# Kernel tuning notes

Hardware: AMD Instinct MI355X
Metric: run time of the kernel (lower is better)

The kernel has to match this reference:

```python
import jax, jax.numpy as jnp
import numpy as np

B, H, W, C = 16, 56, 56, 384
WS, SHIFT, NH = 8, 4, 12
HID = 4 * C
N = WS * WS
EPS = 1e-5


def _rel_index():
    coords = np.stack(np.meshgrid(np.arange(WS), np.arange(WS), indexing='ij')).reshape(2, -1)
    rel = coords[:, :, None] - coords[:, None, :]
    rel = rel.transpose(1, 2, 0).astype(np.int32)
    rel[..., 0] += WS - 1
    rel[..., 1] += WS - 1
    rel[..., 0] *= 2 * WS - 1
    return rel.sum(-1)  # [N, N]


def _attn_mask():
    img = np.zeros((H, W))
    bounds = [(0, H - WS), (H - WS, H - SHIFT), (H - SHIFT, H)]
    cnt = 0
    for h0, h1 in bounds:
        for w0, w1 in bounds:
            img[h0:h1, w0:w1] = cnt
            cnt += 1
    mw = img.reshape(H // WS, WS, W // WS, WS).transpose(0, 2, 1, 3).reshape(-1, N)
    am = mw[:, None, :] - mw[:, :, None]
    return np.where(am != 0, -100.0, 0.0).astype(np.float32)  # [nW, N, N]


def setup_inputs() -> dict:
    key = jax.random.key(0)
    ks = jax.random.split(key, 12)
    s = lambda k, shp, sc=0.02: (jax.random.normal(k, shp, jnp.float32) * sc)
    return {
        'x': jax.random.normal(ks[0], (B, H * W, C), jnp.float32),
        'norm1_g': jnp.ones((C,), jnp.float32),
        'norm1_b': jnp.zeros((C,), jnp.float32),
        'qkv_w': s(ks[1], (C, 3 * C)),
        'qkv_b': jnp.zeros((3 * C,), jnp.float32),
        'proj_w': s(ks[2], (C, C)),
        'proj_b': jnp.zeros((C,), jnp.float32),
        'rel_bias': s(ks[3], ((2 * WS - 1) * (2 * WS - 1), NH)),
        'norm2_g': jnp.ones((C,), jnp.float32),
        'norm2_b': jnp.zeros((C,), jnp.float32),
        'fc1_w': s(ks[4], (C, HID)),
        'fc1_b': jnp.zeros((HID,), jnp.float32),
        'fc2_w': s(ks[5], (HID, C)),
        'fc2_b': jnp.zeros((C,), jnp.float32),
        'rel_index': jnp.asarray(_rel_index()),
        'attn_mask': jnp.asarray(_attn_mask()),
    }


def _ln(x, g, b):
    mu = x.mean(-1, keepdims=True)
    var = ((x - mu) ** 2).mean(-1, keepdims=True)
    return (x - mu) * jax.lax.rsqrt(var + EPS) * g + b


def reference(x, norm1_g, norm1_b, qkv_w, qkv_b, proj_w, proj_b, rel_bias,
              norm2_g, norm2_b, fc1_w, fc1_b, fc2_w, fc2_b, rel_index, attn_mask):
    hd = C // NH
    scale = hd ** -0.5
    shortcut = x
    h = _ln(x, norm1_g, norm1_b).reshape(B, H, W, C)
    h = jnp.roll(h, (-SHIFT, -SHIFT), axis=(1, 2))
    # window partition -> [B*nW, N, C]
    xw = h.reshape(B, H // WS, WS, W // WS, WS, C).transpose(0, 1, 3, 2, 4, 5).reshape(-1, N, C)
    B_ = xw.shape[0]
    qkv = (xw @ qkv_w + qkv_b).reshape(B_, N, 3, NH, hd).transpose(2, 0, 3, 1, 4)
    q, k, v = qkv[0], qkv[1], qkv[2]  # [B_, NH, N, hd]
    attn = jnp.einsum('bhid,bhjd->bhij', q * scale, k)
    bias = rel_bias[rel_index.reshape(-1)].reshape(N, N, NH).transpose(2, 0, 1)  # [NH, N, N]
    attn = attn + bias[None]
    nW = attn_mask.shape[0]
    attn = attn.reshape(B_ // nW, nW, NH, N, N) + attn_mask[None, :, None]
    attn = attn.reshape(B_, NH, N, N)
    attn = jax.nn.softmax(attn, axis=-1)
    out = jnp.einsum('bhij,bhjd->bhid', attn, v).transpose(0, 2, 1, 3).reshape(B_, N, C)
    out = out @ proj_w + proj_b
    # window reverse
    out = out.reshape(B, H // WS, W // WS, WS, WS, C).transpose(0, 1, 3, 2, 4, 5).reshape(B, H, W, C)
    out = jnp.roll(out, (SHIFT, SHIFT), axis=(1, 2)).reshape(B, H * W, C)
    y = shortcut + out
    h2 = _ln(y, norm2_g, norm2_b)
    mlp = jax.nn.gelu(h2 @ fc1_w + fc1_b, approximate=False) @ fc2_w + fc2_b
    y = y + mlp
    return (y, attn)
```

## Files before the change

kernel.cpp:

```cpp
#include <hip/hip_runtime.h>
#include <hip/hip_bf16.h>
#include <math.h>

#define ROWS 50176

typedef short s16;
typedef unsigned int u32;
typedef __attribute__((ext_vector_type(4))) float f32x4;
typedef __attribute__((ext_vector_type(8))) short s16x8;
typedef __attribute__((ext_vector_type(8))) __bf16 bf16x8;

typedef __attribute__((address_space(1))) const u32 gu32;
typedef __attribute__((address_space(3))) u32 lu32;

__device__ __forceinline__ void gload16(const void* g, void* l) {
  __builtin_amdgcn_global_load_lds((gu32*)g, (lu32*)l, 16, 0, 0);
}

__device__ __forceinline__ s16 f2bf(float f) {
  unsigned u = __float_as_uint(f);
  u = (u + 0x7fffu + ((u >> 16) & 1u)) >> 16;
  return (s16)u;
}

__global__ void convT(const float* __restrict__ src, s16* __restrict__ dst, int K, int N) {
  int i = blockIdx.x * 256 + threadIdx.x;
  if (i >= K * N) return;
  int n = i / K, k = i - n * K;
  dst[i] = f2bf(src[(size_t)k * N + n]);
}

__global__ __launch_bounds__(256) void ln_k(const float* __restrict__ x,
    const float* __restrict__ g, const float* __restrict__ b,
    s16* __restrict__ out, int window_map) {
  int r = blockIdx.x * 4 + (threadIdx.x >> 6);
  int lane = threadIdx.x & 63;
  size_t src;
  if (window_map) {
    int w = r >> 6, t = r & 63;
    int bb = w / 49, wi = w - bb * 49;
    int wh = wi / 7, ww = wi - wh * 7;
    int i = (wh * 8 + (t >> 3) + 4) % 56;
    int j = (ww * 8 + (t & 7) + 4) % 56;
    src = (size_t)bb * 3136 + i * 56 + j;
  } else {
    src = (size_t)r;
  }
  const float* xr = x + src * 384;
  float v[6];
  float s = 0.f;
#pragma unroll
  for (int e = 0; e < 6; ++e) { v[e] = xr[lane + e * 64]; s += v[e]; }
#pragma unroll
  for (int o = 1; o < 64; o <<= 1) s += __shfl_xor(s, o, 64);
  float mu = s * (1.f / 384.f);
  float q = 0.f;
#pragma unroll
  for (int e = 0; e < 6; ++e) { float d = v[e] - mu; q += d * d; }
#pragma unroll
  for (int o = 1; o < 64; o <<= 1) q += __shfl_xor(q, o, 64);
  float rs = rsqrtf(q * (1.f / 384.f) + 1e-5f);
  s16* orow = out + (size_t)r * 384;
#pragma unroll
  for (int e = 0; e < 6; ++e) {
    int c = lane + e * 64;
    orow[c] = f2bf((v[e] - mu) * rs * g[c] + b[c]);
  }
}

template<int EPI>
__global__ __launch_bounds__(256) void gemm_bt(const s16* __restrict__ A,
    const s16* __restrict__ BT, const float* __restrict__ bias, int K, int N,
    s16* __restrict__ obf, float* of, const float* res) {
  __shared__ s16 Asm[128 * 64];
  __shared__ s16 Bsm[128 * 64];
  const int t = threadIdx.x;
  const int nbx = N >> 7;
  const int nwg = gridDim.x;
  {
  }
  int id = blockIdx.x;
  const int q8 = nwg >> 3, r8 = nwg & 7;
  const int xcd = id & 7, loc = id >> 3;
  const int swz = (xcd < r8 ? xcd * (q8 + 1) : r8 * (q8 + 1) + (xcd - r8) * q8) + loc;
  const int by = swz / nbx, bx = swz - by * nbx;
  const int m0 = by * 128, n0 = bx * 128;

  const int wv = t >> 6, lane = t & 63;
  const int wr = wv >> 1, wc = wv & 1;
  const int lr = lane & 15, lg = lane >> 4;

  const s16* asrc[4]; const s16* bsrc[4];
  char* adst[4]; char* bdst[4];
#pragma unroll
  for (int i = 0; i < 4; ++i) {
    int o = (i * 256 + t) * 16;
    int row = o >> 7, pc = (o >> 4) & 7, lc = pc ^ (row & 7);
    asrc[i] = A + (size_t)(m0 + row) * K + lc * 8;
    adst[i] = (char*)Asm + o;
    bsrc[i] = BT + (size_t)(n0 + row) * K + lc * 8;
    bdst[i] = (char*)Bsm + o;
  }

  f32x4 acc[4][4] = {};

  for (int k0 = 0; k0 < K; k0 += 64) {
#pragma unroll
    for (int i = 0; i < 4; ++i) {
      gload16(asrc[i] + k0, adst[i]);
      gload16(bsrc[i] + k0, bdst[i]);
    }
    __syncthreads();
    bf16x8 af[2][4], bv[2][4];
#pragma unroll
    for (int kk = 0; kk < 2; ++kk) {
      const int cb = ((kk << 2) | lg) ^ (lr & 7);
#pragma unroll
      for (int m = 0; m < 4; ++m) {
        af[kk][m] = *reinterpret_cast<const bf16x8*>(
            (const char*)Asm + (wr * 64 + m * 16 + lr) * 128 + cb * 16);
        bv[kk][m] = *reinterpret_cast<const bf16x8*>(
            (const char*)Bsm + (wc * 64 + m * 16 + lr) * 128 + cb * 16);
      }
    }
#pragma unroll
    for (int kk = 0; kk < 2; ++kk)
#pragma unroll
      for (int m = 0; m < 4; ++m)
#pragma unroll
        for (int n = 0; n < 4; ++n)
          acc[m][n] = __builtin_amdgcn_mfma_f32_16x16x32_bf16(af[kk][m], bv[kk][n], acc[m][n], 0, 0, 0);
    __syncthreads();
  }

#pragma unroll
  for (int m = 0; m < 4; ++m) {
#pragma unroll
    for (int r = 0; r < 4; ++r) {
      const int row = m0 + wr * 64 + m * 16 + lg * 4 + r;
      size_t drow = (size_t)row;
      if (EPI == 1) {
        int w = row >> 6, tt = row & 63;
        int bb = w / 49, wi = w - bb * 49;
        int wh = wi / 7, ww = wi - wh * 7;
        int fi = (wh * 8 + (tt >> 3) + 4) % 56;
        int fj = (ww * 8 + (tt & 7) + 4) % 56;
        drow = (size_t)bb * 3136 + fi * 56 + fj;
      }
#pragma unroll
      for (int n = 0; n < 4; ++n) {
        const int col = n0 + wc * 64 + n * 16 + lr;
        float v = acc[m][n][r] + bias[col];
        if (EPI == 0) {
          obf[(size_t)row * N + col] = f2bf(v);
        } else if (EPI == 1) {
          size_t o = drow * 384 + col;
          of[o] = res[o] + v;
        } else if (EPI == 2) {
          v = 0.5f * v * (1.f + erff(v * 0.70710678118f));
          obf[(size_t)row * N + col] = f2bf(v);
        } else {
          size_t o = (size_t)row * 384 + col;
          of[o] = res[o] + v;
        }
      }
    }
  }
}

__global__ __launch_bounds__(64) void attn_k(const s16* __restrict__ qkv,
    const float* __restrict__ rel_bias, const int* __restrict__ rel_index,
    const float* __restrict__ mask, float* __restrict__ probs, s16* __restrict__ aout) {
  __shared__ s16 VT[32][72];
  __shared__ s16 P[64][72];
  const int blk = blockIdx.x;
  const int w = blk / 12, nh = blk - w * 12;
  const int lane = threadIdx.x;
  const int lr = lane & 15, lg = lane >> 4;
  const s16* base = qkv + (size_t)w * 64 * 1152;

  {
    const s16* vrow = base + (size_t)lane * 1152 + 768 + nh * 32;
    s16x8 v0 = *reinterpret_cast<const s16x8*>(vrow);
    s16x8 v1 = *reinterpret_cast<const s16x8*>(vrow + 8);
    s16x8 v2 = *reinterpret_cast<const s16x8*>(vrow + 16);
    s16x8 v3 = *reinterpret_cast<const s16x8*>(vrow + 24);
#pragma unroll
    for (int d = 0; d < 8; ++d) {
      VT[d][lane] = v0[d];
      VT[8 + d][lane] = v1[d];
      VT[16 + d][lane] = v2[d];
      VT[24 + d][lane] = v3[d];
    }
  }

  bf16x8 qf[4], kf[4];
#pragma unroll
  for (int m = 0; m < 4; ++m)
    qf[m] = *reinterpret_cast<const bf16x8*>(base + (size_t)(m * 16 + lr) * 1152 + nh * 32 + lg * 8);
#pragma unroll
  for (int n = 0; n < 4; ++n)
    kf[n] = *reinterpret_cast<const bf16x8*>(base + (size_t)(n * 16 + lr) * 1152 + 384 + nh * 32 + lg * 8);

  f32x4 s[4][4] = {};
#pragma unroll
  for (int m = 0; m < 4; ++m)
#pragma unroll
    for (int n = 0; n < 4; ++n)
      s[m][n] = __builtin_amdgcn_mfma_f32_16x16x32_bf16(qf[m], kf[n], s[m][n], 0, 0, 0);

  const float scale = 0.1767766952966369f;
  const float* mrow = mask + (size_t)(w % 49) * 4096;
#pragma unroll
  for (int m = 0; m < 4; ++m)
#pragma unroll
    for (int n = 0; n < 4; ++n)
#pragma unroll
      for (int r = 0; r < 4; ++r) {
        int i = m * 16 + lg * 4 + r, j = n * 16 + lr;
        s[m][n][r] = s[m][n][r] * scale
                   + rel_bias[(size_t)rel_index[i * 64 + j] * 12 + nh]
                   + mrow[i * 64 + j];
      }
#pragma unroll
  for (int m = 0; m < 4; ++m)
#pragma unroll
    for (int r = 0; r < 4; ++r) {
      float mx = fmaxf(fmaxf(s[m][0][r], s[m][1][r]), fmaxf(s[m][2][r], s[m][3][r]));
#pragma unroll
      for (int o = 1; o < 16; o <<= 1) mx = fmaxf(mx, __shfl_xor(mx, o, 64));
      float sum = 0.f;
#pragma unroll
      for (int n = 0; n < 4; ++n) {
        float e = __expf(s[m][n][r] - mx);
        s[m][n][r] = e;
        sum += e;
      }
#pragma unroll
      for (int o = 1; o < 16; o <<= 1) sum += __shfl_xor(sum, o, 64);
      float inv = 1.f / sum;
#pragma unroll
      for (int n = 0; n < 4; ++n) s[m][n][r] *= inv;
    }
  float* prow = probs + (size_t)(w * 12 + nh) * 4096;
#pragma unroll
  for (int m = 0; m < 4; ++m)
#pragma unroll
    for (int n = 0; n < 4; ++n)
#pragma unroll
      for (int r = 0; r < 4; ++r) {
        int i = m * 16 + lg * 4 + r, j = n * 16 + lr;
        float pv = s[m][n][r];
        prow[i * 64 + j] = pv;
        P[i][j] = f2bf(pv);
      }
  __syncthreads();
  f32x4 o2[4][2] = {};
#pragma unroll
  for (int m = 0; m < 4; ++m)
#pragma unroll
    for (int kk = 0; kk < 2; ++kk) {
      bf16x8 pa = *reinterpret_cast<const bf16x8*>(&P[m * 16 + lr][kk * 32 + lg * 8]);
#pragma unroll
      for (int n = 0; n < 2; ++n) {
        bf16x8 vb = *reinterpret_cast<const bf16x8*>(&VT[n * 16 + lr][kk * 32 + lg * 8]);
        o2[m][n] = __builtin_amdgcn_mfma_f32_16x16x32_bf16(pa, vb, o2[m][n], 0, 0, 0);
      }
    }
#pragma unroll
  for (int m = 0; m < 4; ++m)
#pragma unroll
    for (int n = 0; n < 2; ++n)
#pragma unroll
      for (int r = 0; r < 4; ++r) {
        int i = m * 16 + lg * 4 + r, d = n * 16 + lr;
        aout[((size_t)w * 64 + i) * 384 + nh * 32 + d] = f2bf(o2[m][n][r]);
      }
}

extern "C" void kernel_launch(void* const* d_in, const int* in_sizes, int n_in,
                              void* d_out, int out_size, void* d_ws, size_t ws_size,
                              hipStream_t stream) {
  const float* x        = (const float*)d_in[0];
  const float* n1g      = (const float*)d_in[1];
  const float* n1b      = (const float*)d_in[2];
  const float* qkv_w    = (const float*)d_in[3];
  const float* qkv_b    = (const float*)d_in[4];
  const float* proj_w   = (const float*)d_in[5];
  const float* proj_b   = (const float*)d_in[6];
  const float* rel_bias = (const float*)d_in[7];
  const float* n2g      = (const float*)d_in[8];
  const float* n2b      = (const float*)d_in[9];
  const float* fc1_w    = (const float*)d_in[10];
  const float* fc1_b    = (const float*)d_in[11];
  const float* fc2_w    = (const float*)d_in[12];
  const float* fc2_b    = (const float*)d_in[13];
  const int*   rel_idx  = (const int*)d_in[14];
  const float* amask    = (const float*)d_in[15];

  float* out   = (float*)d_out;
  float* probs = out + (size_t)ROWS * 384;

  s16* wqkvT = (s16*)d_ws;
  s16* wprojT = wqkvT + 1152 * 384;
  s16* wfc1T = wprojT + 384 * 384;
  s16* wfc2T = wfc1T + 1536 * 384;
  s16* bufA = wfc2T + 384 * 1536;
  s16* bufB = bufA + (size_t)ROWS * 384;
  s16* bufC = bufB + (size_t)ROWS * 1152;

  convT<<<(1152 * 384) / 256, 256, 0, stream>>>(qkv_w, wqkvT, 384, 1152);
  convT<<<(384 * 384) / 256, 256, 0, stream>>>(proj_w, wprojT, 384, 384);
  convT<<<(1536 * 384) / 256, 256, 0, stream>>>(fc1_w, wfc1T, 384, 1536);
  convT<<<(384 * 1536) / 256, 256, 0, stream>>>(fc2_w, wfc2T, 1536, 384);

  ln_k<<<ROWS / 4, 256, 0, stream>>>(x, n1g, n1b, bufA, 1);
  gemm_bt<0><<<(1152 / 128) * (ROWS / 128), 256, 0, stream>>>(bufA, wqkvT, qkv_b, 384, 1152, bufB, nullptr, nullptr);
  attn_k<<<784 * 12, 64, 0, stream>>>(bufB, rel_bias, rel_idx, amask, probs, bufC);
  gemm_bt<1><<<(384 / 128) * (ROWS / 128), 256, 0, stream>>>(bufC, wprojT, proj_b, 384, 384, nullptr, out, x);
  ln_k<<<ROWS / 4, 256, 0, stream>>>(out, n2g, n2b, bufA, 0);
  gemm_bt<2><<<(1536 / 128) * (ROWS / 128), 256, 0, stream>>>(bufA, wfc1T, fc1_b, 384, 1536, bufB, nullptr, nullptr);
  gemm_bt<3><<<(384 / 128) * (ROWS / 128), 256, 0, stream>>>(bufB, wfc2T, fc2_b, 1536, 384, nullptr, out, out);
}
```

Baseline: 547.8 us.

## Double-buffer LDS tiles in GEMM to overlap global loads with MFMA

The shared-memory tiles of the bf16 GEMM become two ping-pong buffers. The loads for the next K-step are issued before computing the current one, and a partial vmcnt wait lets those in-flight loads overlap with the MFMA work. This aims to hide global-to-LDS latency that was previously exposed at each iteration. In exchange, LDS use doubles to 64KB per block, which may reduce occupancy, and correctness now depends on manual waitcnt and barrier placement.

New measurement: 568.1 us. +3.7%, slower.

```diff
diff --git a/kernel.cpp b/kernel.cpp
--- a/kernel.cpp
+++ b/kernel.cpp
@@ -72,13 +72,10 @@
 __global__ __launch_bounds__(256) void gemm_bt(const s16* __restrict__ A,
     const s16* __restrict__ BT, const float* __restrict__ bias, int K, int N,
     s16* __restrict__ obf, float* of, const float* res) {
-  __shared__ s16 Asm[128 * 64];
-  __shared__ s16 Bsm[128 * 64];
+  __shared__ s16 smem[2][2][128 * 64];
   const int t = threadIdx.x;
   const int nbx = N >> 7;
   const int nwg = gridDim.x;
-  {
-  }
   int id = blockIdx.x;
   const int q8 = nwg >> 3, r8 = nwg & 7;
   const int xcd = id & 7, loc = id >> 3;
@@ -91,36 +88,51 @@
   const int lr = lane & 15, lg = lane >> 4;
 
   const s16* asrc[4]; const s16* bsrc[4];
-  char* adst[4]; char* bdst[4];
+  int dofs[4];
 #pragma unroll
   for (int i = 0; i < 4; ++i) {
     int o = (i * 256 + t) * 16;
     int row = o >> 7, pc = (o >> 4) & 7, lc = pc ^ (row & 7);
+    dofs[i] = o;
     asrc[i] = A + (size_t)(m0 + row) * K + lc * 8;
-    adst[i] = (char*)Asm + o;
     bsrc[i] = BT + (size_t)(n0 + row) * K + lc * 8;
-    bdst[i] = (char*)Bsm + o;
   }
 
   f32x4 acc[4][4] = {};
 
+#pragma unroll
+  for (int i = 0; i < 4; ++i) {
+    gload16(asrc[i], (char*)&smem[0][0][0] + dofs[i]);
+    gload16(bsrc[i], (char*)&smem[0][1][0] + dofs[i]);
+  }
+
+  int cur = 0;
   for (int k0 = 0; k0 < K; k0 += 64) {
-#pragma unroll
-    for (int i = 0; i < 4; ++i) {
-      gload16(asrc[i] + k0, adst[i]);
-      gload16(bsrc[i] + k0, bdst[i]);
-    }
-    __syncthreads();
+    if (k0 + 64 < K) {
+#pragma unroll
+      for (int i = 0; i < 4; ++i) {
+        gload16(asrc[i] + k0 + 64, (char*)&smem[cur ^ 1][0][0] + dofs[i]);
+        gload16(bsrc[i] + k0 + 64, (char*)&smem[cur ^ 1][1][0] + dofs[i]);
+      }
+      __builtin_amdgcn_sched_barrier(0);
+      asm volatile("s_waitcnt vmcnt(8)" ::: "memory");
+    } else {
+      __builtin_amdgcn_sched_barrier(0);
+      asm volatile("s_waitcnt vmcnt(0)" ::: "memory");
+    }
+    __builtin_amdgcn_s_barrier();
+    __builtin_amdgcn_sched_barrier(0);
+
+    const char* Ab = (const char*)&smem[cur][0][0];
+    const char* Bb = (const char*)&smem[cur][1][0];
     bf16x8 af[2][4], bv[2][4];
 #pragma unroll
     for (int kk = 0; kk < 2; ++kk) {
       const int cb = ((kk << 2) | lg) ^ (lr & 7);
 #pragma unroll
       for (int m = 0; m < 4; ++m) {
-        af[kk][m] = *reinterpret_cast<const bf16x8*>(
-            (const char*)Asm + (wr * 64 + m * 16 + lr) * 128 + cb * 16);
-        bv[kk][m] = *reinterpret_cast<const bf16x8*>(
-            (const char*)Bsm + (wc * 64 + m * 16 + lr) * 128 + cb * 16);
+        af[kk][m] = *reinterpret_cast<const bf16x8*>(Ab + (wr * 64 + m * 16 + lr) * 128 + cb * 16);
+        bv[kk][m] = *reinterpret_cast<const bf16x8*>(Bb + (wc * 64 + m * 16 + lr) * 128 + cb * 16);
       }
     }
 #pragma unroll
@@ -130,7 +142,10 @@
 #pragma unroll
         for (int n = 0; n < 4; ++n)
           acc[m][n] = __builtin_amdgcn_mfma_f32_16x16x32_bf16(af[kk][m], bv[kk][n], acc[m][n], 0, 0, 0);
-    __syncthreads();
+    __builtin_amdgcn_sched_barrier(0);
+    __builtin_amdgcn_s_barrier();
+    __builtin_amdgcn_sched_barrier(0);
+    cur ^= 1;
   }
 
 #pragma unroll
```
